# Performance work log

Measured on AMD Instinct MI355X. Metric: run time of the kernel, lower is better.

Reference implementation:

```python
import jax, jax.numpy as jnp
import numpy as np

N_HEADS = 16
WINDOW_SIZE = 128


def setup_inputs() -> dict:
    key = jax.random.key(0)
    ks = jax.random.split(key, 5)
    B, T, D = 2, 2048, 1024
    x = jax.random.normal(ks[0], (B, T, D), dtype=jnp.float32)
    w_qkv = jax.random.normal(ks[1], (3 * D, D), dtype=jnp.float32) * (D ** -0.5)
    b_qkv = jax.random.normal(ks[2], (3 * D,), dtype=jnp.float32) * 0.01
    w_out = jax.random.normal(ks[3], (D, D), dtype=jnp.float32) * (D ** -0.5)
    b_out = jax.random.normal(ks[4], (D,), dtype=jnp.float32) * 0.01
    return {"x": x, "w_qkv": w_qkv, "b_qkv": b_qkv, "w_out": w_out, "b_out": b_out}


def reference(x, w_qkv, b_qkv, w_out, b_out):
    B, T, D = x.shape
    H = N_HEADS
    hd = D // H
    scale = hd ** -0.5

    # qkv projection: (B,T,3D) -> (3,B,H,T,hd)
    qkv = (x @ w_qkv.T + b_qkv).reshape(B, T, 3, H, hd)
    qkv = jnp.transpose(qkv, (2, 0, 3, 1, 4))
    q, k, v = qkv[0], qkv[1], qkv[2]

    pos = jnp.arange(T)
    # mask[i, j]: |j - i| <= w/2 and j >= i  (faithful to original, which
    # due to its index orientation allows query i to attend to keys j >= i)
    mask = (jnp.abs(pos[None, :] - pos[:, None]) <= WINDOW_SIZE // 2) & (
        pos[None, :] >= pos[:, None]
    )

    attn = jnp.einsum("bhqd,bhkd->bhqk", q, k) * scale  # (B,H,T,T)
    attn = jnp.where(mask[None, None], attn, -jnp.inf)
    attn = jax.nn.softmax(attn, axis=-1)
    attn = jnp.nan_to_num(attn, nan=0.0)

    out = jnp.einsum("bhqk,bhkd->bhqd", attn, v)  # (B,H,T,hd)
    out = jnp.transpose(out, (0, 2, 1, 3)).reshape(B, T, D)
    return out @ w_out.T + b_out
```

## Files before the change

### kernel.cpp

```cpp
#include <hip/hip_runtime.h>
#include <hip/hip_bf16.h>
#include <stdint.h>


typedef short bf16x8 __attribute__((ext_vector_type(8)));
typedef float f32x4 __attribute__((ext_vector_type(4)));

typedef const __attribute__((address_space(1))) void* gptr_t;
typedef __attribute__((address_space(3))) void* lptr_t;

__device__ __forceinline__ float bf2f(short u) {
    union { float f; uint32_t i; } x;
    x.i = ((uint32_t)(uint16_t)u) << 16;
    return x.f;
}
__device__ __forceinline__ short f2bf(float f) {
    __hip_bfloat16 h = __float2bfloat16(f);
    return *reinterpret_cast<short*>(&h);
}

__global__ __launch_bounds__(256)
void convert_all(const float* __restrict__ x, const float* __restrict__ wq,
                 const float* __restrict__ bq, const float* __restrict__ wo,
                 const float* __restrict__ bo,
                 short* __restrict__ xb, short* __restrict__ wqb, short* __restrict__ bqb,
                 short* __restrict__ wob, short* __restrict__ bob) {
    int i = blockIdx.x * 256 + threadIdx.x;
    const float* src; short* dst; int o;
    if      (i <  524288) { src = x;  dst = xb;  o = i; }
    else if (i <  917504) { src = wq; dst = wqb; o = i - 524288; }
    else if (i <  917888) { src = bq; dst = bqb; o = i - 917504; }
    else if (i < 1048960) { src = wo; dst = wob; o = i - 917888; }
    else if (i < 1049088) { src = bo; dst = bob; o = i - 1048960; }
    else return;
    const int e = o * 8;
    float4 a = *(const float4*)(src + e);
    float4 b = *(const float4*)(src + e + 4);
    short t[8];
    t[0] = f2bf(a.x); t[1] = f2bf(a.y); t[2] = f2bf(a.z); t[3] = f2bf(a.w);
    t[4] = f2bf(b.x); t[5] = f2bf(b.y); t[6] = f2bf(b.z); t[7] = f2bf(b.w);
    *(uint4*)(dst + e) = *(const uint4*)t;
}

template <bool OUT_F32>
__global__ __launch_bounds__(256)
void gemm_bt_bias(const short* __restrict__ A, const short* __restrict__ Bt,
                  const short* __restrict__ bias, void* __restrict__ Cv,
                  int M, int N, int K) {
    __shared__ short As[128 * 32];
    __shared__ short Bs[128 * 32];

    const int tid  = threadIdx.x;
    const int lane = tid & 63;
    const int w    = tid >> 6;
    const int quad = lane >> 4;
    const int l16  = lane & 15;
    const int wm   = w >> 1;
    const int wn   = w & 1;
    const int mBase = blockIdx.y * 128;
    const int nBase = blockIdx.x * 128;

    f32x4 acc[4][4] = {};

    const int nK = K >> 5;
    for (int kt = 0; kt < nK; ++kt) {
        const int kb = kt << 5;
#pragma unroll
        for (int i = 0; i < 2; ++i) {
            const int e   = i * 2048 + tid * 8;
            const int row = e >> 5;
            const int col = e & 31;
            const short* ga = A  + (size_t)(mBase + row) * K + kb + col;
            const short* gb = Bt + (size_t)(nBase + row) * K + kb + col;
            lptr_t la = (lptr_t)(As + i * 2048 + w * 512);
            lptr_t lb = (lptr_t)(Bs + i * 2048 + w * 512);
            __builtin_amdgcn_global_load_lds((gptr_t)ga, la, 16, 0, 0);
            __builtin_amdgcn_global_load_lds((gptr_t)gb, lb, 16, 0, 0);
        }
        __syncthreads();

        bf16x8 af[4], bfr[4];
#pragma unroll
        for (int mi = 0; mi < 4; ++mi)
            af[mi] = *(const bf16x8*)(As + (wm * 64 + mi * 16 + l16) * 32 + quad * 8);
#pragma unroll
        for (int ni = 0; ni < 4; ++ni)
            bfr[ni] = *(const bf16x8*)(Bs + (wn * 64 + ni * 16 + l16) * 32 + quad * 8);
#pragma unroll
        for (int mi = 0; mi < 4; ++mi)
#pragma unroll
            for (int ni = 0; ni < 4; ++ni)
                acc[mi][ni] = __builtin_amdgcn_mfma_f32_16x16x32_bf16(
                    af[mi], bfr[ni], acc[mi][ni], 0, 0, 0);
        __syncthreads();
    }

#pragma unroll
    for (int ni = 0; ni < 4; ++ni) {
        const int n = nBase + wn * 64 + ni * 16 + l16;
        const float bv = bf2f(bias[n]);
#pragma unroll
        for (int mi = 0; mi < 4; ++mi)
#pragma unroll
            for (int r = 0; r < 4; ++r) {
                const int m = mBase + wm * 64 + mi * 16 + quad * 4 + r;
                if (OUT_F32) ((float*)Cv)[(size_t)m * N + n] = acc[mi][ni][r] + bv;
                else         ((short*)Cv)[(size_t)m * N + n] = f2bf(acc[mi][ni][r] + bv);
            }
    }
}

__global__ __launch_bounds__(256)
void attn_mfma(const short* __restrict__ qkv, short* __restrict__ attn_out, int B, int T) {
    __shared__ short k_s[128 * 72];
    __shared__ short v_s[144 * 66];
    __shared__ short p_s[64 * 104];

    const int tid  = threadIdx.x;
    const int lane = tid & 63;
    const int w    = tid >> 6;
    const int qd   = lane >> 4;
    const int l16  = lane & 15;
    const int qs   = blockIdx.x * 64;
    const int h    = blockIdx.y;
    const int b    = blockIdx.z;
    const size_t rs   = 3072;
    const size_t base = (size_t)b * T * rs;
    const int qoff = h * 64, koff = 1024 + h * 64, voff = 2048 + h * 64;

#pragma unroll
    for (int i = 0; i < 5; ++i) {
        const int c   = tid + i * 256;
        const int row = c >> 3;
        if (row >= 144) break;
        const int ch = (c & 7) * 8;
        int gr = qs + row; if (gr > T - 1) gr = T - 1;
        uint4 uv = *(const uint4*)(qkv + base + (size_t)gr * rs + voff + ch);
        if (row < 128) {
            uint4 uk = *(const uint4*)(qkv + base + (size_t)gr * rs + koff + ch);
            *(uint4*)&k_s[row * 72 + ch] = uk;
        }
        const uint32_t* vp = (const uint32_t*)&uv;
        uint32_t* vd = (uint32_t*)&v_s[row * 66 + ch];
        vd[0] = vp[0]; vd[1] = vp[1]; vd[2] = vp[2]; vd[3] = vp[3];
    }
    __syncthreads();

    bf16x8 aq0, aq1;
    {
        const short* g = qkv + base + (size_t)(qs + 16 * w + l16) * rs + qoff + qd * 8;
        aq0 = *(const bf16x8*)(g);
        aq1 = *(const bf16x8*)(g + 32);
    }

    f32x4 sacc[5] = {};
#pragma unroll
    for (int u = 0; u < 5; ++u) {
        const int krow = 16 * (w + u) + l16;
        bf16x8 bk0 = *(const bf16x8*)&k_s[krow * 72 + qd * 8];
        bf16x8 bk1 = *(const bf16x8*)&k_s[krow * 72 + 32 + qd * 8];
        sacc[u] = __builtin_amdgcn_mfma_f32_16x16x32_bf16(aq0, bk0, sacc[u], 0, 0, 0);
        sacc[u] = __builtin_amdgcn_mfma_f32_16x16x32_bf16(aq1, bk1, sacc[u], 0, 0, 0);
    }

    const float scale = 0.125f;
    float pw[5][4];
    float inv[4];
#pragma unroll
    for (int r = 0; r < 4; ++r) {
        const int m = 4 * qd + r;
        float mx = -3.4e38f;
#pragma unroll
        for (int u = 0; u < 5; ++u) {
            const int rel = 16 * u + l16 - m;
            const int j   = qs + 16 * (w + u) + l16;
            const bool ok = (rel >= 0) & (rel <= 64) & (j < T);
            const float v = ok ? sacc[u][r] * scale : -3.4e38f;
            pw[u][r] = v;
            mx = fmaxf(mx, v);
        }
#pragma unroll
        for (int msk = 1; msk <= 8; msk <<= 1) mx = fmaxf(mx, __shfl_xor(mx, msk));
        float sum = 0.f;
#pragma unroll
        for (int u = 0; u < 5; ++u) {
            float e = (pw[u][r] <= -3.0e38f) ? 0.f : __expf(pw[u][r] - mx);
            pw[u][r] = e;
            sum += e;
        }
#pragma unroll
        for (int msk = 1; msk <= 8; msk <<= 1) sum += __shfl_xor(sum, msk);
        inv[r] = 1.0f / sum;
    }

#pragma unroll
    for (int u = 0; u < 5; ++u)
#pragma unroll
        for (int r = 0; r < 4; ++r)
            p_s[(16 * w + 4 * qd + r) * 104 + 16 * u + l16] = f2bf(pw[u][r]);
#pragma unroll
    for (int r = 0; r < 4; ++r)
        p_s[(16 * w + 4 * qd + r) * 104 + 80 + l16] = 0;

    f32x4 oacc[4] = {};
#pragma unroll
    for (int ks = 0; ks < 3; ++ks) {
        bf16x8 ap = *(const bf16x8*)&p_s[(16 * w + l16) * 104 + ks * 32 + qd * 8];
#pragma unroll
        for (int dt = 0; dt < 4; ++dt) {
            short t[8];
#pragma unroll
            for (int j = 0; j < 8; ++j)
                t[j] = v_s[(16 * w + ks * 32 + qd * 8 + j) * 66 + 16 * dt + l16];
            bf16x8 bv = *(const bf16x8*)t;
            oacc[dt] = __builtin_amdgcn_mfma_f32_16x16x32_bf16(ap, bv, oacc[dt], 0, 0, 0);
        }
    }

#pragma unroll
    for (int dt = 0; dt < 4; ++dt)
#pragma unroll
        for (int r = 0; r < 4; ++r) {
            const size_t row = (size_t)(b * T + qs + 16 * w + 4 * qd + r);
            attn_out[row * 1024 + h * 64 + 16 * dt + l16] = f2bf(oacc[dt][r] * inv[r]);
        }
}

extern "C" void kernel_launch(void* const* d_in, const int* in_sizes, int n_in,
                              void* d_out, int out_size, void* d_ws, size_t ws_size,
                              hipStream_t stream) {
    (void)in_sizes; (void)n_in; (void)out_size; (void)ws_size;
    const int B = 2, T = 2048, D = 1024;
    const int M = B * T;

    char* ws = (char*)d_ws;
    size_t off = 0;
    short* xb   = (short*)(ws + off); off += (size_t)M * D * 2;
    short* wqkb = (short*)(ws + off); off += (size_t)3 * D * D * 2;
    short* bqkb = (short*)(ws + off); off += (size_t)3 * D * 2;
    short* wob  = (short*)(ws + off); off += (size_t)D * D * 2;
    short* bob  = (short*)(ws + off); off += (size_t)D * 2;
    short* qkv  = (short*)(ws + off); off += (size_t)M * 3 * D * 2;
    short* attn = (short*)(ws + off); off += (size_t)M * D * 2;

    convert_all<<<dim3(4099), 256, 0, stream>>>(
        (const float*)d_in[0], (const float*)d_in[1], (const float*)d_in[2],
        (const float*)d_in[3], (const float*)d_in[4], xb, wqkb, bqkb, wob, bob);

    gemm_bt_bias<false><<<dim3(3 * D / 128, M / 128), 256, 0, stream>>>(
        xb, wqkb, bqkb, qkv, M, 3 * D, D);
    attn_mfma<<<dim3(T / 64, 16, B), 256, 0, stream>>>(qkv, attn, B, T);
    gemm_bt_bias<true><<<dim3(D / 128, M / 128), 256, 0, stream>>>(
        attn, wob, bob, d_out, M, D, D);
}
```

Baseline: 162.9 us.

## Swap MFMA operands for vectorized row-contiguous stores and shrink out-projection tile

```diff
diff --git a/kernel.cpp b/kernel.cpp
--- a/kernel.cpp
+++ b/kernel.cpp
@@ -42,18 +42,17 @@
     *(uint4*)(dst + e) = *(const uint4*)t;
 }
 
-template <bool OUT_F32>
 __global__ __launch_bounds__(256)
-void gemm_bt_bias(const short* __restrict__ A, const short* __restrict__ Bt,
-                  const short* __restrict__ bias, void* __restrict__ Cv,
-                  int M, int N, int K) {
+void gemm_bt_128(const short* __restrict__ A, const short* __restrict__ Bt,
+                 const short* __restrict__ bias, short* __restrict__ C,
+                 int M, int N, int K) {
     __shared__ short As[128 * 32];
     __shared__ short Bs[128 * 32];
 
     const int tid  = threadIdx.x;
     const int lane = tid & 63;
     const int w    = tid >> 6;
-    const int quad = lane >> 4;
+    const int qd   = lane >> 4;
     const int l16  = lane & 15;
     const int wm   = w >> 1;
     const int wn   = w & 1;
@@ -82,31 +81,107 @@
         bf16x8 af[4], bfr[4];
 #pragma unroll
         for (int mi = 0; mi < 4; ++mi)
-            af[mi] = *(const bf16x8*)(As + (wm * 64 + mi * 16 + l16) * 32 + quad * 8);
+            af[mi] = *(const bf16x8*)(As + (wm * 64 + mi * 16 + l16) * 32 + qd * 8);
 #pragma unroll
         for (int ni = 0; ni < 4; ++ni)
-            bfr[ni] = *(const bf16x8*)(Bs + (wn * 64 + ni * 16 + l16) * 32 + quad * 8);
+            bfr[ni] = *(const bf16x8*)(Bs + (wn * 64 + ni * 16 + l16) * 32 + qd * 8);
 #pragma unroll
         for (int mi = 0; mi < 4; ++mi)
 #pragma unroll
             for (int ni = 0; ni < 4; ++ni)
                 acc[mi][ni] = __builtin_amdgcn_mfma_f32_16x16x32_bf16(
-                    af[mi], bfr[ni], acc[mi][ni], 0, 0, 0);
+                    bfr[ni], af[mi], acc[mi][ni], 0, 0, 0);
         __syncthreads();
     }
 
 #pragma unroll
     for (int ni = 0; ni < 4; ++ni) {
-        const int n = nBase + wn * 64 + ni * 16 + l16;
-        const float bv = bf2f(bias[n]);
-#pragma unroll
-        for (int mi = 0; mi < 4; ++mi)
-#pragma unroll
-            for (int r = 0; r < 4; ++r) {
-                const int m = mBase + wm * 64 + mi * 16 + quad * 4 + r;
-                if (OUT_F32) ((float*)Cv)[(size_t)m * N + n] = acc[mi][ni][r] + bv;
-                else         ((short*)Cv)[(size_t)m * N + n] = f2bf(acc[mi][ni][r] + bv);
-            }
+        const int n0 = nBase + wn * 64 + ni * 16 + qd * 4;
+        float bv[4];
+#pragma unroll
+        for (int r = 0; r < 4; ++r) bv[r] = bf2f(bias[n0 + r]);
+#pragma unroll
+        for (int mi = 0; mi < 4; ++mi) {
+            const int m = mBase + wm * 64 + mi * 16 + l16;
+            short t[4];
+#pragma unroll
+            for (int r = 0; r < 4; ++r) t[r] = f2bf(acc[mi][ni][r] + bv[r]);
+            *(uint2*)&C[(size_t)m * N + n0] = *(const uint2*)t;
+        }
+    }
+}
+
+__global__ __launch_bounds__(256)
+void gemm_bt_64(const short* __restrict__ A, const short* __restrict__ Bt,
+                const short* __restrict__ bias, float* __restrict__ C,
+                int M, int N, int K) {
+    __shared__ short As[64 * 32];
+    __shared__ short Bs[128 * 32];
+
+    const int tid  = threadIdx.x;
+    const int lane = tid & 63;
+    const int w    = tid >> 6;
+    const int qd   = lane >> 4;
+    const int l16  = lane & 15;
+    const int wm   = w >> 1;
+    const int wn   = w & 1;
+    const int mBase = blockIdx.y * 64;
+    const int nBase = blockIdx.x * 128;
+
+    f32x4 acc[2][4] = {};
+
+    const int nK = K >> 5;
+    for (int kt = 0; kt < nK; ++kt) {
+        const int kb = kt << 5;
+        {
+            const int e   = tid * 8;
+            const int row = e >> 5;
+            const int col = e & 31;
+            const short* ga = A + (size_t)(mBase + row) * K + kb + col;
+            lptr_t la = (lptr_t)(As + w * 512);
+            __builtin_amdgcn_global_load_lds((gptr_t)ga, la, 16, 0, 0);
+        }
+#pragma unroll
+        for (int i = 0; i < 2; ++i) {
+            const int e   = i * 2048 + tid * 8;
+            const int row = e >> 5;
+            const int col = e & 31;
+            const short* gb = Bt + (size_t)(nBase + row) * K + kb + col;
+            lptr_t lb = (lptr_t)(Bs + i * 2048 + w * 512);
+            __builtin_amdgcn_global_load_lds((gptr_t)gb, lb, 16, 0, 0);
+        }
+        __syncthreads();
+
+        bf16x8 af[2], bfr[4];
+#pragma unroll
+        for (int mi = 0; mi < 2; ++mi)
+            af[mi] = *(const bf16x8*)(As + (wm * 32 + mi * 16 + l16) * 32 + qd * 8);
+#pragma unroll
+        for (int ni = 0; ni < 4; ++ni)
+            bfr[ni] = *(const bf16x8*)(Bs + (wn * 64 + ni * 16 + l16) * 32 + qd * 8);
+#pragma unroll
+        for (int mi = 0; mi < 2; ++mi)
+#pragma unroll
+            for (int ni = 0; ni < 4; ++ni)
+                acc[mi][ni] = __builtin_amdgcn_mfma_f32_16x16x32_bf16(
+                    bfr[ni], af[mi], acc[mi][ni], 0, 0, 0);
+        __syncthreads();
+    }
+
+#pragma unroll
+    for (int ni = 0; ni < 4; ++ni) {
+        const int n0 = nBase + wn * 64 + ni * 16 + qd * 4;
+        float bv[4];
+#pragma unroll
+        for (int r = 0; r < 4; ++r) bv[r] = bf2f(bias[n0 + r]);
+#pragma unroll
+        for (int mi = 0; mi < 2; ++mi) {
+            const int m = mBase + wm * 32 + mi * 16 + l16;
+            f32x4 o;
+#pragma unroll
+            for (int r = 0; r < 4; ++r) o[r] = acc[mi][ni][r] + bv[r];
+            *(f32x4*)&C[(size_t)m * N + n0] = o;
+        }
     }
 }
 
@@ -197,7 +272,7 @@
     for (int u = 0; u < 5; ++u)
 #pragma unroll
         for (int r = 0; r < 4; ++r)
-            p_s[(16 * w + 4 * qd + r) * 104 + 16 * u + l16] = f2bf(pw[u][r]);
+            p_s[(16 * w + 4 * qd + r) * 104 + 16 * u + l16] = f2bf(pw[u][r] * inv[r]);
 #pragma unroll
     for (int r = 0; r < 4; ++r)
         p_s[(16 * w + 4 * qd + r) * 104 + 80 + l16] = 0;
@@ -213,17 +288,18 @@
             for (int j = 0; j < 8; ++j)
                 t[j] = v_s[(16 * w + ks * 32 + qd * 8 + j) * 66 + 16 * dt + l16];
             bf16x8 bv = *(const bf16x8*)t;
-            oacc[dt] = __builtin_amdgcn_mfma_f32_16x16x32_bf16(ap, bv, oacc[dt], 0, 0, 0);
-        }
-    }
-
-#pragma unroll
-    for (int dt = 0; dt < 4; ++dt)
-#pragma unroll
-        for (int r = 0; r < 4; ++r) {
-            const size_t row = (size_t)(b * T + qs + 16 * w + 4 * qd + r);
-            attn_out[row * 1024 + h * 64 + 16 * dt + l16] = f2bf(oacc[dt][r] * inv[r]);
-        }
+            oacc[dt] = __builtin_amdgcn_mfma_f32_16x16x32_bf16(bv, ap, oacc[dt], 0, 0, 0);
+        }
+    }
+
+    const size_t row = (size_t)(b * T + qs + 16 * w + l16);
+#pragma unroll
+    for (int dt = 0; dt < 4; ++dt) {
+        short t[4];
+#pragma unroll
+        for (int r = 0; r < 4; ++r) t[r] = f2bf(oacc[dt][r]);
+        *(uint2*)&attn_out[row * 1024 + h * 64 + dt * 16 + qd * 4] = *(const uint2*)t;
+    }
 }
 
 extern "C" void kernel_launch(void* const* d_in, const int* in_sizes, int n_in,
@@ -247,9 +323,9 @@
         (const float*)d_in[0], (const float*)d_in[1], (const float*)d_in[2],
         (const float*)d_in[3], (const float*)d_in[4], xb, wqkb, bqkb, wob, bob);
 
-    gemm_bt_bias<false><<<dim3(3 * D / 128, M / 128), 256, 0, stream>>>(
+    gemm_bt_128<<<dim3(3 * D / 128, M / 128), 256, 0, stream>>>(
         xb, wqkb, bqkb, qkv, M, 3 * D, D);
     attn_mfma<<<dim3(T / 64, 16, B), 256, 0, stream>>>(qkv, attn, B, T);
-    gemm_bt_bias<true><<<dim3(D / 128, M / 128), 256, 0, stream>>>(
-        attn, wob, bob, d_out, M, D, D);
-}
+    gemm_bt_64<<<dim3(D / 128, M / 64), 256, 0, stream>>>(
+        attn, wob, bob, (float*)d_out, M, D, D);
+}
```

Result: no change. 164.5 us (+1.0%).

## Double GEMM K-tile to 64, smaller M tile for output GEMM, vectorize attn stores

Applied to the files above, without the earlier changes.

```diff
diff --git a/kernel.cpp b/kernel.cpp
--- a/kernel.cpp
+++ b/kernel.cpp
@@ -42,56 +42,68 @@
     *(uint4*)(dst + e) = *(const uint4*)t;
 }
 
-template <bool OUT_F32>
+template <int BM, bool OUT_F32>
 __global__ __launch_bounds__(256)
-void gemm_bt_bias(const short* __restrict__ A, const short* __restrict__ Bt,
-                  const short* __restrict__ bias, void* __restrict__ Cv,
-                  int M, int N, int K) {
-    __shared__ short As[128 * 32];
-    __shared__ short Bs[128 * 32];
+void gemm_bt(const short* __restrict__ A, const short* __restrict__ Bt,
+             const short* __restrict__ bias, void* __restrict__ Cv,
+             int M, int N, int K) {
+    __shared__ short As[BM * 64];
+    __shared__ short Bs[128 * 64];
+    constexpr int NMI = BM / 32;
 
     const int tid  = threadIdx.x;
     const int lane = tid & 63;
     const int w    = tid >> 6;
-    const int quad = lane >> 4;
+    const int qd   = lane >> 4;
     const int l16  = lane & 15;
     const int wm   = w >> 1;
     const int wn   = w & 1;
-    const int mBase = blockIdx.y * 128;
+    const int mBase = blockIdx.y * BM;
     const int nBase = blockIdx.x * 128;
-
-    f32x4 acc[4][4] = {};
-
-    const int nK = K >> 5;
+    const int lr = lane >> 2;
+    const int lc = (lane & 3) * 8;
+
+    f32x4 acc[NMI][4] = {};
+
+    const int nK = K >> 6;
     for (int kt = 0; kt < nK; ++kt) {
-        const int kb = kt << 5;
-#pragma unroll
-        for (int i = 0; i < 2; ++i) {
-            const int e   = i * 2048 + tid * 8;
-            const int row = e >> 5;
-            const int col = e & 31;
-            const short* ga = A  + (size_t)(mBase + row) * K + kb + col;
-            const short* gb = Bt + (size_t)(nBase + row) * K + kb + col;
-            lptr_t la = (lptr_t)(As + i * 2048 + w * 512);
-            lptr_t lb = (lptr_t)(Bs + i * 2048 + w * 512);
+        const int kb = kt << 6;
+#pragma unroll
+        for (int j = 0; j < BM / 32; ++j) {
+            const int c  = w * (BM / 32) + j;
+            const int kk = c & 1, r0 = (c >> 1) * 16;
+            const short* ga = A + (size_t)(mBase + r0 + lr) * K + kb + kk * 32 + lc;
+            lptr_t la = (lptr_t)(As + kk * (BM * 32) + r0 * 32);
             __builtin_amdgcn_global_load_lds((gptr_t)ga, la, 16, 0, 0);
+        }
+#pragma unroll
+        for (int j = 0; j < 4; ++j) {
+            const int c  = w * 4 + j;
+            const int kk = c & 1, r0 = (c >> 1) * 16;
+            const short* gb = Bt + (size_t)(nBase + r0 + lr) * K + kb + kk * 32 + lc;
+            lptr_t lb = (lptr_t)(Bs + kk * 4096 + r0 * 32);
             __builtin_amdgcn_global_load_lds((gptr_t)gb, lb, 16, 0, 0);
         }
         __syncthreads();
 
-        bf16x8 af[4], bfr[4];
-#pragma unroll
-        for (int mi = 0; mi < 4; ++mi)
-            af[mi] = *(const bf16x8*)(As + (wm * 64 + mi * 16 + l16) * 32 + quad * 8);
-#pragma unroll
-        for (int ni = 0; ni < 4; ++ni)
-            bfr[ni] = *(const bf16x8*)(Bs + (wn * 64 + ni * 16 + l16) * 32 + quad * 8);
-#pragma unroll
-        for (int mi = 0; mi < 4; ++mi)
+#pragma unroll
+        for (int kk = 0; kk < 2; ++kk) {
+            bf16x8 af[NMI], bfr[4];
+#pragma unroll
+            for (int mi = 0; mi < NMI; ++mi)
+                af[mi] = *(const bf16x8*)(As + kk * (BM * 32) +
+                          (wm * (BM / 2) + mi * 16 + l16) * 32 + qd * 8);
 #pragma unroll
             for (int ni = 0; ni < 4; ++ni)
-                acc[mi][ni] = __builtin_amdgcn_mfma_f32_16x16x32_bf16(
-                    af[mi], bfr[ni], acc[mi][ni], 0, 0, 0);
+                bfr[ni] = *(const bf16x8*)(Bs + kk * 4096 +
+                          (wn * 64 + ni * 16 + l16) * 32 + qd * 8);
+#pragma unroll
+            for (int mi = 0; mi < NMI; ++mi)
+#pragma unroll
+                for (int ni = 0; ni < 4; ++ni)
+                    acc[mi][ni] = __builtin_amdgcn_mfma_f32_16x16x32_bf16(
+                        af[mi], bfr[ni], acc[mi][ni], 0, 0, 0);
+        }
         __syncthreads();
     }
 
@@ -100,10 +112,10 @@
         const int n = nBase + wn * 64 + ni * 16 + l16;
         const float bv = bf2f(bias[n]);
 #pragma unroll
-        for (int mi = 0; mi < 4; ++mi)
+        for (int mi = 0; mi < NMI; ++mi)
 #pragma unroll
             for (int r = 0; r < 4; ++r) {
-                const int m = mBase + wm * 64 + mi * 16 + quad * 4 + r;
+                const int m = mBase + wm * (BM / 2) + mi * 16 + qd * 4 + r;
                 if (OUT_F32) ((float*)Cv)[(size_t)m * N + n] = acc[mi][ni][r] + bv;
                 else         ((short*)Cv)[(size_t)m * N + n] = f2bf(acc[mi][ni][r] + bv);
             }
@@ -197,7 +209,7 @@
     for (int u = 0; u < 5; ++u)
 #pragma unroll
         for (int r = 0; r < 4; ++r)
-            p_s[(16 * w + 4 * qd + r) * 104 + 16 * u + l16] = f2bf(pw[u][r]);
+            p_s[(16 * w + 4 * qd + r) * 104 + 16 * u + l16] = f2bf(pw[u][r] * inv[r]);
 #pragma unroll
     for (int r = 0; r < 4; ++r)
         p_s[(16 * w + 4 * qd + r) * 104 + 80 + l16] = 0;
@@ -213,17 +225,18 @@
             for (int j = 0; j < 8; ++j)
                 t[j] = v_s[(16 * w + ks * 32 + qd * 8 + j) * 66 + 16 * dt + l16];
             bf16x8 bv = *(const bf16x8*)t;
-            oacc[dt] = __builtin_amdgcn_mfma_f32_16x16x32_bf16(ap, bv, oacc[dt], 0, 0, 0);
-        }
-    }
-
-#pragma unroll
-    for (int dt = 0; dt < 4; ++dt)
-#pragma unroll
-        for (int r = 0; r < 4; ++r) {
-            const size_t row = (size_t)(b * T + qs + 16 * w + 4 * qd + r);
-            attn_out[row * 1024 + h * 64 + 16 * dt + l16] = f2bf(oacc[dt][r] * inv[r]);
-        }
+            oacc[dt] = __builtin_amdgcn_mfma_f32_16x16x32_bf16(bv, ap, oacc[dt], 0, 0, 0);
+        }
+    }
+
+    const size_t row = (size_t)(b * T + qs + 16 * w + l16);
+#pragma unroll
+    for (int dt = 0; dt < 4; ++dt) {
+        short t[4];
+#pragma unroll
+        for (int r = 0; r < 4; ++r) t[r] = f2bf(oacc[dt][r]);
+        *(uint2*)&attn_out[row * 1024 + h * 64 + dt * 16 + qd * 4] = *(const uint2*)t;
+    }
 }
 
 extern "C" void kernel_launch(void* const* d_in, const int* in_sizes, int n_in,
@@ -247,9 +260,9 @@
         (const float*)d_in[0], (const float*)d_in[1], (const float*)d_in[2],
         (const float*)d_in[3], (const float*)d_in[4], xb, wqkb, bqkb, wob, bob);
 
-    gemm_bt_bias<false><<<dim3(3 * D / 128, M / 128), 256, 0, stream>>>(
+    gemm_bt<128, false><<<dim3(3 * D / 128, M / 128), 256, 0, stream>>>(
         xb, wqkb, bqkb, qkv, M, 3 * D, D);
     attn_mfma<<<dim3(T / 64, 16, B), 256, 0, stream>>>(qkv, attn, B, T);
-    gemm_bt_bias<true><<<dim3(D / 128, M / 128), 256, 0, stream>>>(
+    gemm_bt<64, true><<<dim3(D / 128, M / 64), 256, 0, stream>>>(
         attn, wob, bob, d_out, M, D, D);
 }
```

Result: no change. 162.2 us (-0.4%).
